# Kernel tuning notes

Hardware: AMD Instinct MI355X
Metric: run time of the kernel (lower is better)

The kernel has to match this reference:

```python
import jax, jax.numpy as jnp
import numpy as np

B, S, DIM, LW, CHUNK = 4, 4096, 512, 512, 64


def _l2n(x):
    n = jnp.sqrt(jnp.sum(x * x, axis=-1, keepdims=True))
    return x / jnp.maximum(n, 1e-12)


def setup_inputs() -> dict:
    key = jax.random.key(0)
    k = jax.random.split(key, 10)
    s = 1.0 / np.sqrt(DIM)
    return {
        "x": jax.random.normal(k[0], (B, S, DIM), jnp.float32),
        "Wq": jax.random.normal(k[1], (DIM, DIM), jnp.float32) * s,
        "Wk": jax.random.normal(k[2], (DIM, DIM), jnp.float32) * s,
        "Wv": jax.random.normal(k[3], (DIM, DIM), jnp.float32) * s,
        "init_w1": jax.random.normal(k[4], (LW, DIM), jnp.float32) * 0.02,
        "init_b1": jnp.zeros((LW,), jnp.float32),
        "init_w2": jax.random.normal(k[5], (DIM, LW), jnp.float32) * 0.02,
        "init_b2": jnp.zeros((DIM,), jnp.float32),
        "alpha_w": jax.random.normal(k[6], (DIM,), jnp.float32) * s,
        "alpha_b": jnp.full((1,), -5.0, jnp.float32),
        "eta_w": jax.random.normal(k[7], (DIM,), jnp.float32) * s,
        "eta_b": jnp.full((1,), 2.0, jnp.float32),
        "theta_w": jax.random.normal(k[8], (DIM,), jnp.float32) * s,
        "theta_b": jnp.full((1,), -4.6, jnp.float32),
        "chunk_size": CHUNK,
    }


def reference(x, Wq, Wk, Wv, init_w1, init_b1, init_w2, init_b2,
              alpha_w, alpha_b, eta_w, eta_b, theta_w, theta_b, chunk_size):
    b, s, d = x.shape
    c = int(chunk_size)
    nC = s // c
    lw = init_w1.shape[0]
    # per-sample memory params (broadcast of shared init) + zero momentum
    w1 = jnp.broadcast_to(init_w1, (b, lw, d))
    b1 = jnp.broadcast_to(init_b1, (b, lw))
    w2 = jnp.broadcast_to(init_w2, (b, d, lw))
    b2 = jnp.broadcast_to(init_b2, (b, d))
    mom = (jnp.zeros_like(w1), jnp.zeros_like(b1), jnp.zeros_like(w2), jnp.zeros_like(b2))
    xc = x.reshape(b, nC, c, d).transpose(1, 0, 2, 3)  # [nC, B, C, D]

    def step(carry, x_c):
        (w1, b1, w2, b2), (mw1, mb1, mw2, mb2) = carry
        q = _l2n(x_c @ Wq.T)
        k_ = _l2n(x_c @ Wk.T)
        v = x_c @ Wv.T
        # gates per token -> chunk-averaged, [B]
        a = jax.nn.sigmoid(x_c @ alpha_w + alpha_b).mean(axis=1)
        e = jax.nn.sigmoid(x_c @ eta_w + eta_b).mean(axis=1)
        t = jax.nn.sigmoid(x_c @ theta_w + theta_b).mean(axis=1)
        # retrieval with stale (chunk-constant) memory params
        hq = jax.nn.silu(jnp.einsum('bcd,bhd->bch', q, w1) + b1[:, None, :])
        y = jnp.einsum('bch,bdh->bcd', hq, w2) + b2[:, None, :]
        # per-token grads of mse(mlp(k), v) (mean over feature dim), chunk-averaged.
        # Analytic grads == autodiff of the tiny MLP; avoids [B,C,LW,D] intermediates.
        pre = jnp.einsum('bcd,bhd->bch', k_, w1) + b1[:, None, :]
        sg = jax.nn.sigmoid(pre)
        hk = pre * sg  # silu
        vp = jnp.einsum('bch,bdh->bcd', hk, w2) + b2[:, None, :]
        dvp = 2.0 * (vp - v) / d  # dL/d vp for mse over feature dim
        g_b2 = dvp.mean(axis=1)
        g_w2 = jnp.einsum('bcd,bch->bdh', dvp, hk) / c
        dh = jnp.einsum('bcd,bdh->bch', dvp, w2) * (sg * (1.0 + pre * (1.0 - sg)))
        g_b1 = dh.mean(axis=1)
        g_w1 = jnp.einsum('bch,bcd->bhd', dh, k_) / c
        a3, e3, t3 = a[:, None, None], e[:, None, None], t[:, None, None]
        a2, e2, t2 = a[:, None], e[:, None], t[:, None]
        nmw1 = e3 * mw1 - t3 * g_w1
        nmb1 = e2 * mb1 - t2 * g_b1
        nmw2 = e3 * mw2 - t3 * g_w2
        nmb2 = e2 * mb2 - t2 * g_b2
        nw1 = (1.0 - a3) * w1 + nmw1
        nb1 = (1.0 - a2) * b1 + nmb1
        nw2 = (1.0 - a3) * w2 + nmw2
        nb2 = (1.0 - a2) * b2 + nmb2
        return ((nw1, nb1, nw2, nb2), (nmw1, nmb1, nmw2, nmb2)), y

    _, ys = jax.lax.scan(step, ((w1, b1, w2, b2), mom), xc)
    return ys.transpose(1, 0, 2, 3).reshape(b, s, d)
```

## Files before the change

### kernel.cpp

```cpp
#include <hip/hip_runtime.h>
#include <hip/hip_bf16.h>

#define BB 4
#define SS 4096
#define DD 512
#define LWW 512
#define CC 64
#define NCH 64

typedef unsigned short u16;
using fragAB = __attribute__((ext_vector_type(8))) short;
using fragC  = __attribute__((ext_vector_type(4))) float;
using u16x4  = __attribute__((ext_vector_type(4))) short;

__device__ __forceinline__ short f2bf(float f){
  unsigned u = __float_as_uint(f);
  u = (u + 0x7FFFu + ((u >> 16) & 1u)) >> 16;
  return (short)u;
}
__device__ __forceinline__ float bf2f(short s){
  return __uint_as_float(((unsigned)(u16)s) << 16);
}
__device__ __forceinline__ fragC zeroC(){ fragC z = {0.f,0.f,0.f,0.f}; return z; }

__device__ __forceinline__ fragAB frag_bf16g(const u16* __restrict__ base, int ld, int r0, int k0, int lane){
  return *(const fragAB*)(base + (size_t)(r0 + (lane & 15)) * ld + k0 + ((lane >> 4) << 3));
}
__device__ __forceinline__ fragAB frag_lds(const short* base, int ld, int r0, int k0, int lane){
  return *(const fragAB*)(base + (r0 + (lane & 15)) * ld + k0 + ((lane >> 4) << 3));
}
#define MFMA16(a,b,c) __builtin_amdgcn_mfma_f32_16x16x32_bf16(a,b,c,0,0,0)

__device__ __forceinline__ void ld_sys(fragAB& r, const u16* p){
  asm volatile("global_load_dwordx4 %0, %1, off sc0 sc1" : "=v"(r) : "v"(p) : "memory");
}
__device__ __forceinline__ void st_sys8(u16* p, u16x4 v){
  asm volatile("global_store_dwordx2 %0, %1, off sc0 sc1" :: "v"(p), "v"(v) : "memory");
}
__device__ __forceinline__ void st_sys16(u16* p, fragAB v){
  asm volatile("global_store_dwordx4 %0, %1, off sc0 sc1" :: "v"(p), "v"(v) : "memory");
}
#define WAITVM(N) do { asm volatile("s_waitcnt vmcnt(" #N ")" ::: "memory"); \
                       __builtin_amdgcn_sched_barrier(0); } while (0)

__device__ __forceinline__ const u16* taddr(const u16* base, int c, int kq){
  return base + (((size_t)((kq >> 4)*64 + c)) << 4) + (kq & 15);
}

__device__ __forceinline__ void bar_arrive(unsigned* slots, unsigned phase, int tl){
  asm volatile("s_waitcnt vmcnt(0)" ::: "memory");
  __builtin_amdgcn_sched_barrier(0);
  __syncthreads();
  if (threadIdx.x == 0)
    __hip_atomic_store(slots + (size_t)tl*32, phase, __ATOMIC_RELAXED, __HIP_MEMORY_SCOPE_AGENT);
}
__device__ __forceinline__ void bar_wait(unsigned* slots, unsigned phase){
  if (threadIdx.x < 64){
    bool mine = threadIdx.x < 32;
    unsigned* sp = slots + (size_t)(threadIdx.x & 31)*32;
    for (;;){
      unsigned v = mine ? __hip_atomic_load(sp, __ATOMIC_RELAXED, __HIP_MEMORY_SCOPE_AGENT) : phase;
      if (__all((int)(v >= phase))) break;
      __builtin_amdgcn_s_sleep(1);
    }
  }
  __syncthreads();
}

__global__ __launch_bounds__(256) void k_cvt(const float* __restrict__ x,
    const float* __restrict__ Wq, const float* __restrict__ Wk, const float* __restrict__ Wv,
    u16* __restrict__ xb, u16* __restrict__ Wc, unsigned* __restrict__ bar){
  size_t i = (size_t)blockIdx.x * 256 + threadIdx.x;
  if (blockIdx.x == 0){
    for (int z = threadIdx.x; z < 4096; z += 256) bar[z] = 0u;
  }
  const size_t NX4 = (size_t)BB*SS*DD/4;
  const size_t NW4 = (size_t)DD*DD/4;
  if (i < NX4){
    float4 v = ((const float4*)x)[i];
    u16x4 o = { f2bf(v.x), f2bf(v.y), f2bf(v.z), f2bf(v.w) };
    *(u16x4*)(xb + 4*i) = o;
  } else if (i < NX4 + 3*NW4){
    size_t j = i - NX4;
    const float* src = (j < NW4) ? Wq : (j < 2*NW4) ? Wk : Wv;
    size_t jj = j % NW4;
    float4 v = ((const float4*)src)[jj];
    u16x4 o = { f2bf(v.x), f2bf(v.y), f2bf(v.z), f2bf(v.w) };
    *(u16x4*)(Wc + 4*j) = o;
  }
}

__global__ __launch_bounds__(256) void k_proj(const u16* __restrict__ xb,
    const u16* __restrict__ Wc,
    u16* __restrict__ Qb, u16* __restrict__ Kb, float* __restrict__ V){
  int mt = blockIdx.x / 12, nt = blockIdx.x % 12;
  int lane = threadIdx.x & 63, wid = threadIdx.x >> 6;
  int m0 = mt * 64 + wid * 16;
  const u16* Bp = Wc + (size_t)nt * 128 * DD;
  fragC acc[8];
#pragma unroll
  for (int i = 0; i < 8; ++i) acc[i] = zeroC();
  for (int k0 = 0; k0 < DD; k0 += 32){
    fragAB a = frag_bf16g(xb, DD, m0, k0, lane);
#pragma unroll
    for (int nf = 0; nf < 8; ++nf)
      acc[nf] = MFMA16(a, frag_bf16g(Bp, DD, nf*16, k0, lane), acc[nf]);
  }
#pragma unroll
  for (int nf = 0; nf < 8; ++nf){
#pragma unroll
    for (int r = 0; r < 4; ++r){
      int m = m0 + ((lane >> 4) << 2) + r;
      int col = nt*128 + nf*16 + (lane & 15);
      float v = acc[nf][r];
      if (nt < 4)      Qb[(size_t)m*DD + col]        = (u16)f2bf(v);
      else if (nt < 8) Kb[(size_t)m*DD + col - 512]  = (u16)f2bf(v);
      else             V [(size_t)m*DD + col - 1024] = v;
    }
  }
}

__global__ __launch_bounds__(256) void k_norm(u16* __restrict__ Qb, u16* __restrict__ Kb){
  int idx = blockIdx.x * 4 + (threadIdx.x >> 6);
  int lane = threadIdx.x & 63;
  u16* p = (idx < BB*SS ? Qb + (size_t)idx * DD
                        : Kb + (size_t)(idx - BB*SS) * DD) + lane * 8;
  fragAB v = *(const fragAB*)p;
  float f[8]; float s = 0.f;
#pragma unroll
  for (int i = 0; i < 8; ++i){ f[i] = bf2f(v[i]); s += f[i]*f[i]; }
#pragma unroll
  for (int o = 32; o > 0; o >>= 1) s += __shfl_xor(s, o, 64);
  float inv = 1.f / fmaxf(sqrtf(s), 1e-12f);
  fragAB o8;
#pragma unroll
  for (int i = 0; i < 8; ++i) o8[i] = f2bf(f[i] * inv);
  *(fragAB*)p = o8;
}

__global__ __launch_bounds__(256) void k_trans(const u16* __restrict__ Kb, u16* __restrict__ KT){
  __shared__ short tile[64][68];
  int blk = blockIdx.x;
  int b = blk >> 9, rem = blk & 511;
  int st = rem >> 3, dt = rem & 7;
  int s0 = st*64, d0 = dt*64;
  int sr = threadIdx.x & 63, q = threadIdx.x >> 6;
  const u16* src = Kb + ((size_t)b*SS + s0 + sr)*DD + d0 + q*16;
  fragAB v0 = *(const fragAB*)src;
  fragAB v1 = *(const fragAB*)(src + 8);
#pragma unroll
  for (int i = 0; i < 8; ++i){ tile[sr][q*16+i] = v0[i]; tile[sr][q*16+8+i] = v1[i]; }
  __syncthreads();
  fragAB o0, o1;
#pragma unroll
  for (int i = 0; i < 8; ++i){ o0[i] = tile[q*16+i][sr]; o1[i] = tile[q*16+8+i][sr]; }
  u16* dst = KT + ((size_t)b*DD + d0 + sr)*SS + s0 + q*16;
  *(fragAB*)dst = o0;
  *(fragAB*)(dst + 8) = o1;
}

__global__ __launch_bounds__(256) void k_gates(const float* __restrict__ x,
    const float* __restrict__ aw, const float* __restrict__ ab,
    const float* __restrict__ ew, const float* __restrict__ eb,
    const float* __restrict__ tw, const float* __restrict__ tb,
    float* __restrict__ aet){
  __shared__ float part[64][4][3];
  __shared__ float rowsig[64][3];
  int b = blockIdx.x >> 6, t = blockIdx.x & 63;
  int tid = threadIdx.x;
  int r = tid >> 2, p = tid & 3;
  const float4* xp = (const float4*)(x + ((size_t)b*SS + (size_t)t*CC + r) * DD + p * 128);
  const float4* a4 = (const float4*)(aw + p*128);
  const float4* e4 = (const float4*)(ew + p*128);
  const float4* t4 = (const float4*)(tw + p*128);
  float s0 = 0.f, s1 = 0.f, s2 = 0.f;
  for (int i = 0; i < 32; ++i){
    float4 xv = xp[i], av = a4[i], ev = e4[i], tv = t4[i];
    s0 += xv.x*av.x + xv.y*av.y + xv.z*av.z + xv.w*av.w;
    s1 += xv.x*ev.x + xv.y*ev.y + xv.z*ev.z + xv.w*ev.w;
    s2 += xv.x*tv.x + xv.y*tv.y + xv.z*tv.z + xv.w*tv.w;
  }
  part[r][p][0] = s0; part[r][p][1] = s1; part[r][p][2] = s2;
  __syncthreads();
  if (tid < 64){
    float a_ = part[tid][0][0]+part[tid][1][0]+part[tid][2][0]+part[tid][3][0] + ab[0];
    float e_ = part[tid][0][1]+part[tid][1][1]+part[tid][2][1]+part[tid][3][1] + eb[0];
    float t_ = part[tid][0][2]+part[tid][1][2]+part[tid][2][2]+part[tid][3][2] + tb[0];
    rowsig[tid][0] = 1.f/(1.f+expf(-a_));
    rowsig[tid][1] = 1.f/(1.f+expf(-e_));
    rowsig[tid][2] = 1.f/(1.f+expf(-t_));
  }
  __syncthreads();
  if (tid < 3){
    float s = 0.f;
    for (int i = 0; i < 64; ++i) s += rowsig[i][tid];
    aet[((size_t)b*NCH + t)*3 + tid] = s * (1.f/64.f);
  }
}

__global__ __launch_bounds__(512, 2) void k_scan(
    const u16* __restrict__ Qb, const u16* __restrict__ Kb, const u16* __restrict__ KTg,
    const float* __restrict__ V, const float* __restrict__ aet,
    const float* __restrict__ iw1, const float* __restrict__ ib1,
    const float* __restrict__ iw2, const float* __restrict__ ib2,
    u16* __restrict__ hkb, u16* __restrict__ hqs, u16* __restrict__ hkT,
    u16* __restrict__ dvpb, u16* __restrict__ w2Tb,
    float* __restrict__ out, unsigned* __restrict__ barb)
{
  __shared__ __align__(16) short s_w1[16*520];
  __shared__ __align__(16) short s_w2[16*520];
  __shared__ __align__(16) short s_pf[16*520];
  __shared__ __align__(16) short s_t[16*72];
  __shared__ __align__(16) short s_hk[64*16];
  __shared__ __align__(16) short s_hq[64*16];
  __shared__ float s_part[64][17];
  __shared__ float s_b1[16], s_mb1[16], s_b2[16], s_mb2[16];

  const int tid  = threadIdx.x;
  const int lane = tid & 63;
  const int wid  = tid >> 6;
  const int q    = lane >> 4;
  const int l15  = lane & 15;
  const int qk   = q << 3;
  const int b    = (blockIdx.x & 7) >> 1;
  const int tl   = ((blockIdx.x >> 3) << 1) | (blockIdx.x & 1);
  const int h0   = tl * 16;
  const int d0   = tl * 16;
  unsigned* slots = barb + (size_t)b * 1024;
  unsigned  ph   = 0;

  const u16* Kball = Kb  + (size_t)b*SS*DD;
  const u16* Qball = Qb  + (size_t)b*SS*DD;
  const u16* KTbat = KTg + (size_t)b*DD*SS;
  u16* hk_b  = hkb  + (size_t)b*CC*LWW;
  u16* hq_b  = hqs  + (size_t)b*CC*LWW;
  u16* hkT_b = hkT  + (size_t)b*LWW*CC;
  u16* dv_b  = dvpb + (size_t)b*CC*DD;
  const size_t W2TBUF = (size_t)BB*DD*LWW;

  float w1f[16], mw1f[16], w2f[16], mw2f[16], actr[4];

  {
    u16* w2T0 = w2Tb + (size_t)b*DD*LWW;
#pragma unroll
    for (int nf = 0; nf < 4; ++nf){
      u16x4 pk;
#pragma unroll
      for (int r = 0; r < 4; ++r){
        int hr = q*4 + r;
        int dcol = wid*64 + nf*16 + l15;
        float a = iw1[(size_t)(h0 + hr)*DD + dcol];
        w1f[nf*4+r] = a; mw1f[nf*4+r] = 0.f;
        s_w1[hr*520 + dcol] = f2bf(a);
        float c = iw2[(size_t)(d0 + hr)*LWW + dcol];
        w2f[nf*4+r] = c; mw2f[nf*4+r] = 0.f;
        s_w2[hr*520 + dcol] = f2bf(c);
        pk[r] = f2bf(c);
      }
      st_sys8(w2T0 + (size_t)(wid*64 + nf*16 + l15)*DD + d0 + q*4, pk);
    }
    if (tid < 16){
      s_b1[tid] = ib1[h0 + tid]; s_mb1[tid] = 0.f;
      s_b2[tid] = ib2[d0 + tid]; s_mb2[tid] = 0.f;
    }
#pragma unroll
    for (int r = 0; r < 4; ++r) actr[r] = 0.f;
    WAITVM(0);
    __syncthreads();
  }

  for (int t = 0; t < NCH; ++t){
    if (t > 0){
      fragAB kfr[8];
      {
        const u16* KTm = KTbat + (size_t)(t-1)*CC;
#pragma unroll
        for (int nf = 0; nf < 4; ++nf)
#pragma unroll
          for (int kk = 0; kk < 2; ++kk)
            kfr[nf*2+kk] = frag_bf16g(KTm, SS, wid*64 + nf*16, kk*32, lane);
      }
      {
        const int cst = (wid & 3) * 16;
        const int kh  = (wid >> 2) * 256;
        fragAB fa[8];
        fragC a0 = zeroC();
#pragma unroll
        for (int j = 0; j < 8; ++j) ld_sys(fa[j], taddr(dv_b, cst + l15, kh + j*32 + qk));
        WAITVM(4);
#pragma unroll
        for (int j = 0; j < 4; ++j) a0 = MFMA16(fa[j], frag_lds(s_pf, 520, 0, kh + j*32, lane), a0);
        WAITVM(0);
#pragma unroll
        for (int j = 4; j < 8; ++j) a0 = MFMA16(fa[j], frag_lds(s_pf, 520, 0, kh + j*32, lane), a0);
        if (wid >= 4){
#pragma unroll
          for (int r = 0; r < 4; ++r) s_part[cst + q*4 + r][l15] = a0[r];
        }
        __syncthreads();
        if (wid < 4){
#pragma unroll
          for (int r = 0; r < 4; ++r){
            float v = (a0[r] + s_part[cst + q*4 + r][l15]) * actr[r];
            s_t[l15*72 + cst + q*4 + r] = f2bf(v);
          }
        }
      }
      __syncthreads();
      {
        fragC ag[4];
#pragma unroll
        for (int i = 0; i < 4; ++i) ag[i] = zeroC();
#pragma unroll
        for (int kk = 0; kk < 2; ++kk){
          fragAB af = frag_lds(s_t, 72, 0, kk*32, lane);
#pragma unroll
          for (int nf = 0; nf < 4; ++nf)
            ag[nf] = MFMA16(af, kfr[nf*2+kk], ag[nf]);
        }
        const float* g3 = aet + ((size_t)b*NCH + (t-1)) * 3;
        float ga = g3[0], ge = g3[1], gth = g3[2];
#pragma unroll
        for (int nf = 0; nf < 4; ++nf)
#pragma unroll
          for (int r = 0; r < 4; ++r){
            float g  = ag[nf][r] * (1.f/64.f);
            float m_ = ge*mw1f[nf*4+r] - gth*g;
            float w_ = (1.f-ga)*w1f[nf*4+r] + m_;
            mw1f[nf*4+r] = m_; w1f[nf*4+r] = w_;
            s_w1[(q*4+r)*520 + wid*64 + nf*16 + l15] = f2bf(w_);
          }
        if (tid < 16){
          const fragAB* row = (const fragAB*)(s_t + tid*72);
          float s = 0.f;
#pragma unroll
          for (int j = 0; j < 8; ++j){
            fragAB v = row[j];
#pragma unroll
            for (int i = 0; i < 8; ++i) s += bf2f(v[i]);
          }
          float gb = s * (1.f/64.f);
          float m_ = ge*s_mb1[tid] - gth*gb;
          float bn = (1.f-ga)*s_b1[tid] + m_;
          s_mb1[tid] = m_; s_b1[tid] = bn;
        }
      }
    }
    __syncthreads();
    {
      const u16* Ac = (wid < 4 ? Kball : Qball) + (size_t)t*CC*DD;
      int m0 = (wid & 3) * 16;
      fragC acc = zeroC();
      for (int k0 = 0; k0 < DD; k0 += 32)
        acc = MFMA16(frag_bf16g(Ac, DD, m0, k0, lane),
                     frag_lds(s_w1, 520, 0, k0, lane), acc);
      float bb = s_b1[l15];
      if (wid < 4){
#pragma unroll
        for (int r = 0; r < 4; ++r){
          int c = m0 + q*4 + r;
          float pre = acc[r] + bb;
          float sg  = 1.f/(1.f+expf(-pre));
          float hkv = pre * sg;
          actr[r]   = sg * (1.f + pre * (1.f - sg));
          short hb  = f2bf(hkv);
          s_hk[c*16 + l15] = hb;
          s_t[l15*72 + c]  = hb;
        }
      } else {
#pragma unroll
        for (int r = 0; r < 4; ++r){
          int c = m0 + q*4 + r;
          float hqv = acc[r] + bb;
          float s2  = 1.f/(1.f+expf(-hqv));
          s_hq[c*16 + l15] = f2bf(hqv * s2);
        }
      }
    }
    __syncthreads();
    if (tid < 128){
      st_sys16(hk_b + (size_t)tl*1024 + tid*8, *(const fragAB*)(s_hk + tid*8));
    } else if (tid < 256){
      int i = tid - 128;
      st_sys16(hq_b + (size_t)tl*1024 + i*8, *(const fragAB*)(s_hq + i*8));
    } else if (tid < 384){
      int i = tid - 256;
      int row = i >> 3, seg = i & 7;
      st_sys16(hkT_b + (size_t)(h0 + row)*CC + seg*8, *(const fragAB*)(s_t + row*72 + seg*8));
    }
    ph++; bar_arrive(slots, ph, tl);
    bar_wait(slots, ph);

    {
      const u16* Ah = (wid < 4) ? hq_b : hk_b;
      int m0 = (wid & 3) * 16;
      fragC acc = zeroC();
      fragAB va[4], vb[4], hfr[8];
      float vv[4];
      if (wid >= 4){
#pragma unroll
        for (int r = 0; r < 4; ++r)
          vv[r] = V[((size_t)b*SS + (size_t)t*CC + m0 + q*4 + r)*DD + d0 + l15];
      }
#pragma unroll
      for (int j = 0; j < 4; ++j) ld_sys(va[j], taddr(Ah, m0 + l15, j*32 + qk));
#pragma unroll
      for (int j = 0; j < 4; ++j) ld_sys(vb[j], taddr(Ah, m0 + l15, 128 + j*32 + qk));
      WAITVM(4);
#pragma unroll
      for (int j = 0; j < 4; ++j) acc = MFMA16(va[j], frag_lds(s_w2, 520, 0, j*32, lane), acc);
#pragma unroll
      for (int j = 0; j < 4; ++j) ld_sys(va[j], taddr(Ah, m0 + l15, 256 + j*32 + qk));
      WAITVM(4);
#pragma unroll
      for (int j = 0; j < 4; ++j) acc = MFMA16(vb[j], frag_lds(s_w2, 520, 0, 128 + j*32, lane), acc);
#pragma unroll
      for (int j = 0; j < 4; ++j) ld_sys(vb[j], taddr(Ah, m0 + l15, 384 + j*32 + qk));
      WAITVM(4);
#pragma unroll
      for (int j = 0; j < 4; ++j) acc = MFMA16(va[j], frag_lds(s_w2, 520, 0, 256 + j*32, lane), acc);
#pragma unroll
      for (int nf = 0; nf < 4; ++nf)
#pragma unroll
        for (int kk = 0; kk < 2; ++kk)
          ld_sys(hfr[nf*2+kk], hkT_b + (size_t)(wid*64 + nf*16 + l15)*CC + kk*32 + qk);
      WAITVM(8);
#pragma unroll
      for (int j = 0; j < 4; ++j) acc = MFMA16(vb[j], frag_lds(s_w2, 520, 0, 384 + j*32, lane), acc);

      float bb = s_b2[l15];
      if (wid < 4){
#pragma unroll
        for (int r = 0; r < 4; ++r){
          int c = m0 + q*4 + r;
          __builtin_nontemporal_store(acc[r] + bb,
            &out[((size_t)b*SS + (size_t)t*CC + c)*DD + d0 + l15]);
        }
      } else {
#pragma unroll
        for (int r = 0; r < 4; ++r){
          int c = m0 + q*4 + r;
          float dvv = (acc[r] + bb - vv[r]) * (2.f/512.f);
          short db_ = f2bf(dvv);
          s_hk[c*16 + l15] = db_;
          s_t[l15*72 + c]  = db_;
        }
      }
      __syncthreads();
      if (tid < 128)
        st_sys16(dv_b + (size_t)tl*1024 + tid*8, *(const fragAB*)(s_hk + tid*8));
      ph++; bar_arrive(slots, ph, tl);
      {
        fragC ag[4];
#pragma unroll
        for (int i = 0; i < 4; ++i) ag[i] = zeroC();
#pragma unroll
        for (int kk = 0; kk < 2; ++kk){
          fragAB af = frag_lds(s_t, 72, 0, kk*32, lane);
#pragma unroll
          for (int nf = 0; nf < 4; ++nf)
            ag[nf] = MFMA16(af, hfr[nf*2+kk], ag[nf]);
        }
        fragAB t0, t1;
        int hr = tid >> 5;
        int c0 = (tid & 31) << 4;
        if (t + 1 < NCH){
          const u16* w2Tp = w2Tb + (size_t)(t&1)*W2TBUF + (size_t)b*DD*LWW;
          const u16* src = w2Tp + (size_t)(h0 + hr)*DD + c0;
          ld_sys(t0, src);
          ld_sys(t1, src + 8);
        }
        const float* g3 = aet + ((size_t)b*NCH + t) * 3;
        float ga = g3[0], ge = g3[1], gth = g3[2];
        u16* w2Tn = w2Tb + (size_t)((t+1)&1)*W2TBUF + (size_t)b*DD*LWW;
#pragma unroll
        for (int nf = 0; nf < 4; ++nf){
          u16x4 pk;
#pragma unroll
          for (int r = 0; r < 4; ++r){
            float g  = ag[nf][r] * (1.f/64.f);
            float m_ = ge*mw2f[nf*4+r] - gth*g;
            float w_ = (1.f-ga)*w2f[nf*4+r] + m_;
            mw2f[nf*4+r] = m_; w2f[nf*4+r] = w_;
            short wb = f2bf(w_);
            s_w2[(q*4+r)*520 + wid*64 + nf*16 + l15] = wb;
            pk[r] = wb;
          }
          st_sys8(w2Tn + (size_t)(wid*64 + nf*16 + l15)*DD + d0 + q*4, pk);
        }
        if (tid < 16){
          const fragAB* row = (const fragAB*)(s_t + tid*72);
          float s = 0.f;
#pragma unroll
          for (int j = 0; j < 8; ++j){
            fragAB v = row[j];
#pragma unroll
            for (int i = 0; i < 8; ++i) s += bf2f(v[i]);
          }
          float gb = s * (1.f/64.f);
          float m_ = ge*s_mb2[tid] - gth*gb;
          float bn = (1.f-ga)*s_b2[tid] + m_;
          s_mb2[tid] = m_; s_b2[tid] = bn;
        }
        if (t + 1 < NCH){
          WAITVM(0);
          *(fragAB*)(s_pf + hr*520 + c0)     = t0;
          *(fragAB*)(s_pf + hr*520 + c0 + 8) = t1;
        }
      }
      bar_wait(slots, ph);
    }
  }
}

extern "C" void kernel_launch(void* const* d_in, const int* in_sizes, int n_in,
                              void* d_out, int out_size, void* d_ws, size_t ws_size,
                              hipStream_t stream){
  const float* x   = (const float*)d_in[0];
  const float* Wq  = (const float*)d_in[1];
  const float* Wk  = (const float*)d_in[2];
  const float* Wv  = (const float*)d_in[3];
  const float* iw1 = (const float*)d_in[4];
  const float* ib1 = (const float*)d_in[5];
  const float* iw2 = (const float*)d_in[6];
  const float* ib2 = (const float*)d_in[7];
  const float* aw  = (const float*)d_in[8];
  const float* ab  = (const float*)d_in[9];
  const float* ew  = (const float*)d_in[10];
  const float* eb  = (const float*)d_in[11];
  const float* tw  = (const float*)d_in[12];
  const float* tb  = (const float*)d_in[13];
  float* out = (float*)d_out;

  float* fw = (float*)d_ws;
  float* V    = fw;  fw += (size_t)BB*SS*DD;
  float* aet  = fw;  fw += (size_t)BB*NCH*3 + 64;
  unsigned* bar = (unsigned*)fw; fw += 4096;
  u16* xb   = (u16*)fw;
  u16* Wc   = xb   + (size_t)BB*SS*DD;
  u16* Qb   = Wc   + (size_t)3*DD*DD;
  u16* Kb   = Qb   + (size_t)BB*SS*DD;
  u16* hkb  = Kb   + (size_t)BB*SS*DD;
  u16* hqs  = hkb  + (size_t)BB*CC*LWW;
  u16* hkT  = hqs  + (size_t)BB*CC*LWW;
  u16* dvpb = hkT  + (size_t)BB*LWW*CC;
  u16* w2Tb = dvpb + (size_t)BB*CC*DD;
  u16* KTg  = xb;

  k_cvt  <<<8960, 256, 0, stream>>>(x, Wq, Wk, Wv, xb, Wc, bar);
  k_proj <<<3072, 256, 0, stream>>>(xb, Wc, Qb, Kb, V);
  k_norm <<<8192, 256, 0, stream>>>(Qb, Kb);
  k_trans<<<2048, 256, 0, stream>>>(Kb, KTg);
  k_gates<<<256,  256, 0, stream>>>(x, aw, ab, ew, eb, tw, tb, aet);
  k_scan <<<128,  512, 0, stream>>>(Qb, Kb, KTg, V, aet, iw1, ib1, iw2, ib2,
                                    hkb, hqs, hkT, dvpb, w2Tb, out, bar);
}
```

Before: 1.357 ms.

## Interleave two batches per scan block to hide grid-barrier latency

Each persistent scan block now handles the same hidden/feature tile for two batch elements instead of one, halving the grid to 64 blocks with 1 block per CU. Phases for the two batches are interleaved so that one batch's grid-barrier wait overlaps with the other batch's compute. Weights are duplicated in dynamic shared memory. The trade-off is more registers per thread and fewer blocks to spread across CUs, in exchange for hiding the cross-block synchronisation latency of the sequential scan.

```diff
diff --git a/kernel.cpp b/kernel.cpp
--- a/kernel.cpp
+++ b/kernel.cpp
@@ -7,6 +7,7 @@
 #define LWW 512
 #define CC 64
 #define NCH 64
+#define SCAN_SMEM 111104
 
 typedef unsigned short u16;
 using fragAB = __attribute__((ext_vector_type(8))) short;
@@ -198,7 +199,296 @@
   }
 }
 
-__global__ __launch_bounds__(512, 2) void k_scan(
+struct BCtx {
+  const u16 *Kball, *Qball, *KTbat;
+  u16 *hk_b, *hq_b, *hkT_b, *dv_b, *w2T_b;
+  const float *V_b, *aet_b;
+  float *out_b;
+  unsigned *slots;
+  short *s_w1, *s_w2, *s_pf;
+  float *s_b1, *s_mb1, *s_b2, *s_mb2;
+};
+
+__device__ __forceinline__ void do_init(const BCtx& C,
+    const float* iw1, const float* ib1, const float* iw2, const float* ib2,
+    int tid, int wid, int q, int l15, int h0,
+    float (&w1f)[16], float (&mw1f)[16], float (&w2f)[16], float (&mw2f)[16],
+    float (&actr)[4])
+{
+#pragma unroll
+  for (int nf = 0; nf < 4; ++nf){
+    u16x4 pk;
+#pragma unroll
+    for (int r = 0; r < 4; ++r){
+      int hr = q*4 + r;
+      int dcol = wid*64 + nf*16 + l15;
+      float a = iw1[(size_t)(h0 + hr)*DD + dcol];
+      w1f[nf*4+r] = a; mw1f[nf*4+r] = 0.f;
+      C.s_w1[hr*520 + dcol] = f2bf(a);
+      float c = iw2[(size_t)(h0 + hr)*LWW + dcol];
+      w2f[nf*4+r] = c; mw2f[nf*4+r] = 0.f;
+      C.s_w2[hr*520 + dcol] = f2bf(c);
+      pk[r] = f2bf(c);
+    }
+    st_sys8(C.w2T_b + (size_t)(wid*64 + nf*16 + l15)*DD + h0 + q*4, pk);
+  }
+  if (tid < 16){
+    C.s_b1[tid] = ib1[h0 + tid]; C.s_mb1[tid] = 0.f;
+    C.s_b2[tid] = ib2[h0 + tid]; C.s_mb2[tid] = 0.f;
+  }
+#pragma unroll
+  for (int r = 0; r < 4; ++r) actr[r] = 0.f;
+}
+
+__device__ __forceinline__ void do_phaseA(const BCtx& C, int t,
+    int tid, int lane, int wid, int q, int l15, int qk, int tl, int h0,
+    float (&w1f)[16], float (&mw1f)[16], float (&actr)[4],
+    short* s_t, short* s_hk, short* s_hq, float (*s_part)[17], unsigned phA)
+{
+  if (t > 0){
+    fragAB kfr[8];
+    {
+      const u16* KTm = C.KTbat + (size_t)(t-1)*CC;
+#pragma unroll
+      for (int nf = 0; nf < 4; ++nf)
+#pragma unroll
+        for (int kk = 0; kk < 2; ++kk)
+          kfr[nf*2+kk] = frag_bf16g(KTm, SS, wid*64 + nf*16, kk*32, lane);
+    }
+    {
+      const int cst = (wid & 3) * 16;
+      const int kh  = (wid >> 2) * 256;
+      fragAB fa[8];
+      fragC a0 = zeroC();
+#pragma unroll
+      for (int j = 0; j < 8; ++j) ld_sys(fa[j], taddr(C.dv_b, cst + l15, kh + j*32 + qk));
+      WAITVM(4);
+#pragma unroll
+      for (int j = 0; j < 4; ++j) a0 = MFMA16(fa[j], frag_lds(C.s_pf, 520, 0, kh + j*32, lane), a0);
+      WAITVM(0);
+#pragma unroll
+      for (int j = 4; j < 8; ++j) a0 = MFMA16(fa[j], frag_lds(C.s_pf, 520, 0, kh + j*32, lane), a0);
+      if (wid >= 4){
+#pragma unroll
+        for (int r = 0; r < 4; ++r) s_part[cst + q*4 + r][l15] = a0[r];
+      }
+      __syncthreads();
+      if (wid < 4){
+#pragma unroll
+        for (int r = 0; r < 4; ++r){
+          float v = (a0[r] + s_part[cst + q*4 + r][l15]) * actr[r];
+          s_t[l15*72 + cst + q*4 + r] = f2bf(v);
+        }
+      }
+      __syncthreads();
+    }
+    {
+      fragC ag[4];
+#pragma unroll
+      for (int i = 0; i < 4; ++i) ag[i] = zeroC();
+#pragma unroll
+      for (int kk = 0; kk < 2; ++kk){
+        fragAB af = frag_lds(s_t, 72, 0, kk*32, lane);
+#pragma unroll
+        for (int nf = 0; nf < 4; ++nf)
+          ag[nf] = MFMA16(af, kfr[nf*2+kk], ag[nf]);
+      }
+      const float* g3 = C.aet_b + (size_t)(t-1)*3;
+      float ga = g3[0], ge = g3[1], gth = g3[2];
+#pragma unroll
+      for (int nf = 0; nf < 4; ++nf)
+#pragma unroll
+        for (int r = 0; r < 4; ++r){
+          float g  = ag[nf][r] * (1.f/64.f);
+          float m_ = ge*mw1f[nf*4+r] - gth*g;
+          float w_ = (1.f-ga)*w1f[nf*4+r] + m_;
+          mw1f[nf*4+r] = m_; w1f[nf*4+r] = w_;
+          C.s_w1[(q*4+r)*520 + wid*64 + nf*16 + l15] = f2bf(w_);
+        }
+      if (tid < 16){
+        const fragAB* row = (const fragAB*)(s_t + tid*72);
+        float s = 0.f;
+#pragma unroll
+        for (int j = 0; j < 8; ++j){
+          fragAB v = row[j];
+#pragma unroll
+          for (int i = 0; i < 8; ++i) s += bf2f(v[i]);
+        }
+        float gb = s * (1.f/64.f);
+        float m_ = ge*C.s_mb1[tid] - gth*gb;
+        float bn = (1.f-ga)*C.s_b1[tid] + m_;
+        C.s_mb1[tid] = m_; C.s_b1[tid] = bn;
+      }
+    }
+  }
+  __syncthreads();
+  {
+    const u16* Ac = (wid < 4 ? C.Kball : C.Qball) + (size_t)t*CC*DD;
+    int m0 = (wid & 3) * 16;
+    fragC acc = zeroC();
+    for (int k0 = 0; k0 < DD; k0 += 32)
+      acc = MFMA16(frag_bf16g(Ac, DD, m0, k0, lane),
+                   frag_lds(C.s_w1, 520, 0, k0, lane), acc);
+    float bb = C.s_b1[l15];
+    if (wid < 4){
+#pragma unroll
+      for (int r = 0; r < 4; ++r){
+        int c = m0 + q*4 + r;
+        float pre = acc[r] + bb;
+        float sg  = 1.f/(1.f+expf(-pre));
+        float hkv = pre * sg;
+        actr[r]   = sg * (1.f + pre * (1.f - sg));
+        short hb  = f2bf(hkv);
+        s_hk[c*16 + l15] = hb;
+        s_t[l15*72 + c]  = hb;
+      }
+    } else {
+#pragma unroll
+      for (int r = 0; r < 4; ++r){
+        int c = m0 + q*4 + r;
+        float hqv = acc[r] + bb;
+        float s2  = 1.f/(1.f+expf(-hqv));
+        s_hq[c*16 + l15] = f2bf(hqv * s2);
+      }
+    }
+  }
+  __syncthreads();
+  if (tid < 128){
+    st_sys16(C.hk_b + (size_t)tl*1024 + tid*8, *(const fragAB*)(s_hk + tid*8));
+  } else if (tid < 256){
+    int i = tid - 128;
+    st_sys16(C.hq_b + (size_t)tl*1024 + i*8, *(const fragAB*)(s_hq + i*8));
+  } else if (tid < 384){
+    int i = tid - 256;
+    int row = i >> 3, seg = i & 7;
+    st_sys16(C.hkT_b + (size_t)(h0 + row)*CC + seg*8, *(const fragAB*)(s_t + row*72 + seg*8));
+  }
+  bar_arrive(C.slots, phA, tl);
+}
+
+__device__ __forceinline__ void do_phaseB(const BCtx& C, int t,
+    int tid, int lane, int wid, int q, int l15, int qk, int tl, int d0,
+    float (&w2f)[16], float (&mw2f)[16],
+    short* s_t, short* s_hk, unsigned phB, size_t W2TBUF)
+{
+  const u16* Ah = (wid < 4) ? C.hq_b : C.hk_b;
+  int m0 = (wid & 3) * 16;
+  fragC acc = zeroC();
+  fragAB va[4], vb[4], hfr[8];
+  float vv[4];
+  if (wid >= 4){
+#pragma unroll
+    for (int r = 0; r < 4; ++r)
+      vv[r] = C.V_b[((size_t)t*CC + m0 + q*4 + r)*DD + d0 + l15];
+  }
+#pragma unroll
+  for (int j = 0; j < 4; ++j) ld_sys(va[j], taddr(Ah, m0 + l15, j*32 + qk));
+#pragma unroll
+  for (int j = 0; j < 4; ++j) ld_sys(vb[j], taddr(Ah, m0 + l15, 128 + j*32 + qk));
+  WAITVM(4);
+#pragma unroll
+  for (int j = 0; j < 4; ++j) acc = MFMA16(va[j], frag_lds(C.s_w2, 520, 0, j*32, lane), acc);
+#pragma unroll
+  for (int j = 0; j < 4; ++j) ld_sys(va[j], taddr(Ah, m0 + l15, 256 + j*32 + qk));
+  WAITVM(4);
+#pragma unroll
+  for (int j = 0; j < 4; ++j) acc = MFMA16(vb[j], frag_lds(C.s_w2, 520, 0, 128 + j*32, lane), acc);
+#pragma unroll
+  for (int j = 0; j < 4; ++j) ld_sys(vb[j], taddr(Ah, m0 + l15, 384 + j*32 + qk));
+  WAITVM(4);
+#pragma unroll
+  for (int j = 0; j < 4; ++j) acc = MFMA16(va[j], frag_lds(C.s_w2, 520, 0, 256 + j*32, lane), acc);
+#pragma unroll
+  for (int nf = 0; nf < 4; ++nf)
+#pragma unroll
+    for (int kk = 0; kk < 2; ++kk)
+      ld_sys(hfr[nf*2+kk], C.hkT_b + (size_t)(wid*64 + nf*16 + l15)*CC + kk*32 + qk);
+  WAITVM(8);
+#pragma unroll
+  for (int j = 0; j < 4; ++j) acc = MFMA16(vb[j], frag_lds(C.s_w2, 520, 0, 384 + j*32, lane), acc);
+
+  float bb = C.s_b2[l15];
+  if (wid < 4){
+#pragma unroll
+    for (int r = 0; r < 4; ++r){
+      int c = m0 + q*4 + r;
+      __builtin_nontemporal_store(acc[r] + bb, &C.out_b[((size_t)t*CC + c)*DD + d0 + l15]);
+    }
+  } else {
+#pragma unroll
+    for (int r = 0; r < 4; ++r){
+      int c = m0 + q*4 + r;
+      float dvv = (acc[r] + bb - vv[r]) * (2.f/512.f);
+      short db_ = f2bf(dvv);
+      s_hk[c*16 + l15] = db_;
+      s_t[l15*72 + c]  = db_;
+    }
+  }
+  __syncthreads();
+  if (tid < 128)
+    st_sys16(C.dv_b + (size_t)tl*1024 + tid*8, *(const fragAB*)(s_hk + tid*8));
+  bar_arrive(C.slots, phB, tl);
+  {
+    fragC ag[4];
+#pragma unroll
+    for (int i = 0; i < 4; ++i) ag[i] = zeroC();
+#pragma unroll
+    for (int kk = 0; kk < 2; ++kk){
+      fragAB af = frag_lds(s_t, 72, 0, kk*32, lane);
+#pragma unroll
+      for (int nf = 0; nf < 4; ++nf)
+        ag[nf] = MFMA16(af, hfr[nf*2+kk], ag[nf]);
+    }
+    fragAB t0, t1;
+    int hr = tid >> 5;
+    int c0 = (tid & 31) << 4;
+    if (t + 1 < NCH){
+      const u16* w2Tp = C.w2T_b + (size_t)(t&1)*W2TBUF;
+      const u16* src = w2Tp + (size_t)(d0 + hr)*DD + c0;
+      ld_sys(t0, src);
+      ld_sys(t1, src + 8);
+    }
+    const float* g3 = C.aet_b + (size_t)t*3;
+    float ga = g3[0], ge = g3[1], gth = g3[2];
+    u16* w2Tn = C.w2T_b + (size_t)((t+1)&1)*W2TBUF;
+#pragma unroll
+    for (int nf = 0; nf < 4; ++nf){
+      u16x4 pk;
+#pragma unroll
+      for (int r = 0; r < 4; ++r){
+        float g  = ag[nf][r] * (1.f/64.f);
+        float m_ = ge*mw2f[nf*4+r] - gth*g;
+        float w_ = (1.f-ga)*w2f[nf*4+r] + m_;
+        mw2f[nf*4+r] = m_; w2f[nf*4+r] = w_;
+        short wb = f2bf(w_);
+        C.s_w2[(q*4+r)*520 + wid*64 + nf*16 + l15] = wb;
+        pk[r] = wb;
+      }
+      st_sys8(w2Tn + (size_t)(wid*64 + nf*16 + l15)*DD + d0 + q*4, pk);
+    }
+    if (tid < 16){
+      const fragAB* row = (const fragAB*)(s_t + tid*72);
+      float s = 0.f;
+#pragma unroll
+      for (int j = 0; j < 8; ++j){
+        fragAB v = row[j];
+#pragma unroll
+        for (int i = 0; i < 8; ++i) s += bf2f(v[i]);
+      }
+      float gb = s * (1.f/64.f);
+      float m_ = ge*C.s_mb2[tid] - gth*gb;
+      float bn = (1.f-ga)*C.s_b2[tid] + m_;
+      C.s_mb2[tid] = m_; C.s_b2[tid] = bn;
+    }
+    if (t + 1 < NCH){
+      WAITVM(0);
+      *(fragAB*)(C.s_pf + hr*520 + c0)     = t0;
+      *(fragAB*)(C.s_pf + hr*520 + c0 + 8) = t1;
+    }
+  }
+}
+
+__global__ __launch_bounds__(512, 1) void k_scan(
     const u16* __restrict__ Qb, const u16* __restrict__ Kb, const u16* __restrict__ KTg,
     const float* __restrict__ V, const float* __restrict__ aet,
     const float* __restrict__ iw1, const float* __restrict__ ib1,
@@ -207,14 +497,23 @@
     u16* __restrict__ dvpb, u16* __restrict__ w2Tb,
     float* __restrict__ out, unsigned* __restrict__ barb)
 {
-  __shared__ __align__(16) short s_w1[16*520];
-  __shared__ __align__(16) short s_w2[16*520];
-  __shared__ __align__(16) short s_pf[16*520];
-  __shared__ __align__(16) short s_t[16*72];
-  __shared__ __align__(16) short s_hk[64*16];
-  __shared__ __align__(16) short s_hq[64*16];
-  __shared__ float s_part[64][17];
-  __shared__ float s_b1[16], s_mb1[16], s_b2[16], s_mb2[16];
+  extern __shared__ __align__(16) char smem_raw[];
+  short* sp = (short*)smem_raw;
+  short* s_w1a = sp;               sp += 16*520;
+  short* s_w2a = sp;               sp += 16*520;
+  short* s_pfa = sp;               sp += 16*520;
+  short* s_w1b = sp;               sp += 16*520;
+  short* s_w2b = sp;               sp += 16*520;
+  short* s_pfb = sp;               sp += 16*520;
+  short* s_t   = sp;               sp += 16*72;
+  short* s_hk  = sp;               sp += 64*16;
+  short* s_hq  = sp;               sp += 64*16;
+  float* fb = (float*)sp;
+  float (*s_part)[17] = (float(*)[17])fb;  fb += 64*17;
+  float* s_b1a = fb;  fb += 16;  float* s_mb1a = fb; fb += 16;
+  float* s_b2a = fb;  fb += 16;  float* s_mb2a = fb; fb += 16;
+  float* s_b1b = fb;  fb += 16;  float* s_mb1b = fb; fb += 16;
+  float* s_b2b = fb;  fb += 16;  float* s_mb2b = fb; fb += 16;
 
   const int tid  = threadIdx.x;
   const int lane = tid & 63;
@@ -222,295 +521,56 @@
   const int q    = lane >> 4;
   const int l15  = lane & 15;
   const int qk   = q << 3;
-  const int b    = (blockIdx.x & 7) >> 1;
-  const int tl   = ((blockIdx.x >> 3) << 1) | (blockIdx.x & 1);
+  const int g    = blockIdx.x & 1;
+  const int tl   = blockIdx.x >> 1;
   const int h0   = tl * 16;
-  const int d0   = tl * 16;
-  unsigned* slots = barb + (size_t)b * 1024;
-  unsigned  ph   = 0;
-
-  const u16* Kball = Kb  + (size_t)b*SS*DD;
-  const u16* Qball = Qb  + (size_t)b*SS*DD;
-  const u16* KTbat = KTg + (size_t)b*DD*SS;
-  u16* hk_b  = hkb  + (size_t)b*CC*LWW;
-  u16* hq_b  = hqs  + (size_t)b*CC*LWW;
-  u16* hkT_b = hkT  + (size_t)b*LWW*CC;
-  u16* dv_b  = dvpb + (size_t)b*CC*DD;
+  const int b0   = g*2, b1 = g*2 + 1;
   const size_t W2TBUF = (size_t)BB*DD*LWW;
 
-  float w1f[16], mw1f[16], w2f[16], mw2f[16], actr[4];
-
+  BCtx C0, C1;
   {
-    u16* w2T0 = w2Tb + (size_t)b*DD*LWW;
-#pragma unroll
-    for (int nf = 0; nf < 4; ++nf){
-      u16x4 pk;
-#pragma unroll
-      for (int r = 0; r < 4; ++r){
-        int hr = q*4 + r;
-        int dcol = wid*64 + nf*16 + l15;
-        float a = iw1[(size_t)(h0 + hr)*DD + dcol];
-        w1f[nf*4+r] = a; mw1f[nf*4+r] = 0.f;
-        s_w1[hr*520 + dcol] = f2bf(a);
-        float c = iw2[(size_t)(d0 + hr)*LWW + dcol];
-        w2f[nf*4+r] = c; mw2f[nf*4+r] = 0.f;
-        s_w2[hr*520 + dcol] = f2bf(c);
-        pk[r] = f2bf(c);
-      }
-      st_sys8(w2T0 + (size_t)(wid*64 + nf*16 + l15)*DD + d0 + q*4, pk);
-    }
-    if (tid < 16){
-      s_b1[tid] = ib1[h0 + tid]; s_mb1[tid] = 0.f;
-      s_b2[tid] = ib2[d0 + tid]; s_mb2[tid] = 0.f;
-    }
-#pragma unroll
-    for (int r = 0; r < 4; ++r) actr[r] = 0.f;
-    WAITVM(0);
-    __syncthreads();
-  }
+    C0.Kball = Kb + (size_t)b0*SS*DD;  C1.Kball = Kb + (size_t)b1*SS*DD;
+    C0.Qball = Qb + (size_t)b0*SS*DD;  C1.Qball = Qb + (size_t)b1*SS*DD;
+    C0.KTbat = KTg + (size_t)b0*DD*SS; C1.KTbat = KTg + (size_t)b1*DD*SS;
+    C0.hk_b  = hkb + (size_t)b0*CC*LWW;  C1.hk_b  = hkb + (size_t)b1*CC*LWW;
+    C0.hq_b  = hqs + (size_t)b0*CC*LWW;  C1.hq_b  = hqs + (size_t)b1*CC*LWW;
+    C0.hkT_b = hkT + (size_t)b0*LWW*CC;  C1.hkT_b = hkT + (size_t)b1*LWW*CC;
+    C0.dv_b  = dvpb + (size_t)b0*CC*DD;  C1.dv_b  = dvpb + (size_t)b1*CC*DD;
+    C0.w2T_b = w2Tb + (size_t)b0*DD*LWW; C1.w2T_b = w2Tb + (size_t)b1*DD*LWW;
+    C0.V_b   = V + (size_t)b0*SS*DD;     C1.V_b   = V + (size_t)b1*SS*DD;
+    C0.aet_b = aet + (size_t)b0*NCH*3;   C1.aet_b = aet + (size_t)b1*NCH*3;
+    C0.out_b = out + (size_t)b0*SS*DD;   C1.out_b = out + (size_t)b1*SS*DD;
+    C0.slots = barb + (size_t)b0*1024;   C1.slots = barb + (size_t)b1*1024;
+    C0.s_w1 = s_w1a; C0.s_w2 = s_w2a; C0.s_pf = s_pfa;
+    C1.s_w1 = s_w1b; C1.s_w2 = s_w2b; C1.s_pf = s_pfb;
+    C0.s_b1 = s_b1a; C0.s_mb1 = s_mb1a; C0.s_b2 = s_b2a; C0.s_mb2 = s_mb2a;
+    C1.s_b1 = s_b1b; C1.s_mb1 = s_mb1b; C1.s_b2 = s_b2b; C1.s_mb2 = s_mb2b;
+  }
+
+  float w1f0[16], mw1f0[16], w2f0[16], mw2f0[16], actr0[4];
+  float w1f1[16], mw1f1[16], w2f1[16], mw2f1[16], actr1[4];
+
+  do_init(C0, iw1, ib1, iw2, ib2, tid, wid, q, l15, h0, w1f0, mw1f0, w2f0, mw2f0, actr0);
+  do_init(C1, iw1, ib1, iw2, ib2, tid, wid, q, l15, h0, w1f1, mw1f1, w2f1, mw2f1, actr1);
+  WAITVM(0);
+  __syncthreads();
 
   for (int t = 0; t < NCH; ++t){
-    if (t > 0){
-      fragAB kfr[8];
-      {
-        const u16* KTm = KTbat + (size_t)(t-1)*CC;
-#pragma unroll
-        for (int nf = 0; nf < 4; ++nf)
-#pragma unroll
-          for (int kk = 0; kk < 2; ++kk)
-            kfr[nf*2+kk] = frag_bf16g(KTm, SS, wid*64 + nf*16, kk*32, lane);
-      }
-      {
-        const int cst = (wid & 3) * 16;
-        const int kh  = (wid >> 2) * 256;
-        fragAB fa[8];
-        fragC a0 = zeroC();
-#pragma unroll
-        for (int j = 0; j < 8; ++j) ld_sys(fa[j], taddr(dv_b, cst + l15, kh + j*32 + qk));
-        WAITVM(4);
-#pragma unroll
-        for (int j = 0; j < 4; ++j) a0 = MFMA16(fa[j], frag_lds(s_pf, 520, 0, kh + j*32, lane), a0);
-        WAITVM(0);
-#pragma unroll
-        for (int j = 4; j < 8; ++j) a0 = MFMA16(fa[j], frag_lds(s_pf, 520, 0, kh + j*32, lane), a0);
-        if (wid >= 4){
-#pragma unroll
-          for (int r = 0; r < 4; ++r) s_part[cst + q*4 + r][l15] = a0[r];
-        }
-        __syncthreads();
-        if (wid < 4){
-#pragma unroll
-          for (int r = 0; r < 4; ++r){
-            float v = (a0[r] + s_part[cst + q*4 + r][l15]) * actr[r];
-            s_t[l15*72 + cst + q*4 + r] = f2bf(v);
-          }
-        }
-      }
-      __syncthreads();
-      {
-        fragC ag[4];
-#pragma unroll
-        for (int i = 0; i < 4; ++i) ag[i] = zeroC();
-#pragma unroll
-        for (int kk = 0; kk < 2; ++kk){
-          fragAB af = frag_lds(s_t, 72, 0, kk*32, lane);
-#pragma unroll
-          for (int nf = 0; nf < 4; ++nf)
-            ag[nf] = MFMA16(af, kfr[nf*2+kk], ag[nf]);
-        }
-        const float* g3 = aet + ((size_t)b*NCH + (t-1)) * 3;
-        float ga = g3[0], ge = g3[1], gth = g3[2];
-#pragma unroll
-        for (int nf = 0; nf < 4; ++nf)
-#pragma unroll
-          for (int r = 0; r < 4; ++r){
-            float g  = ag[nf][r] * (1.f/64.f);
-            float m_ = ge*mw1f[nf*4+r] - gth*g;
-            float w_ = (1.f-ga)*w1f[nf*4+r] + m_;
-            mw1f[nf*4+r] = m_; w1f[nf*4+r] = w_;
-            s_w1[(q*4+r)*520 + wid*64 + nf*16 + l15] = f2bf(w_);
-          }
-        if (tid < 16){
-          const fragAB* row = (const fragAB*)(s_t + tid*72);
-          float s = 0.f;
-#pragma unroll
-          for (int j = 0; j < 8; ++j){
-            fragAB v = row[j];
-#pragma unroll
-            for (int i = 0; i < 8; ++i) s += bf2f(v[i]);
-          }
-          float gb = s * (1.f/64.f);
-          float m_ = ge*s_mb1[tid] - gth*gb;
-          float bn = (1.f-ga)*s_b1[tid] + m_;
-          s_mb1[tid] = m_; s_b1[tid] = bn;
-        }
-      }
-    }
-    __syncthreads();
-    {
-      const u16* Ac = (wid < 4 ? Kball : Qball) + (size_t)t*CC*DD;
-      int m0 = (wid & 3) * 16;
-      fragC acc = zeroC();
-      for (int k0 = 0; k0 < DD; k0 += 32)
-        acc = MFMA16(frag_bf16g(Ac, DD, m0, k0, lane),
-                     frag_lds(s_w1, 520, 0, k0, lane), acc);
-      float bb = s_b1[l15];
-      if (wid < 4){
-#pragma unroll
-        for (int r = 0; r < 4; ++r){
-          int c = m0 + q*4 + r;
-          float pre = acc[r] + bb;
-          float sg  = 1.f/(1.f+expf(-pre));
-          float hkv = pre * sg;
-          actr[r]   = sg * (1.f + pre * (1.f - sg));
-          short hb  = f2bf(hkv);
-          s_hk[c*16 + l15] = hb;
-          s_t[l15*72 + c]  = hb;
-        }
-      } else {
-#pragma unroll
-        for (int r = 0; r < 4; ++r){
-          int c = m0 + q*4 + r;
-          float hqv = acc[r] + bb;
-          float s2  = 1.f/(1.f+expf(-hqv));
-          s_hq[c*16 + l15] = f2bf(hqv * s2);
-        }
-      }
-    }
-    __syncthreads();
-    if (tid < 128){
-      st_sys16(hk_b + (size_t)tl*1024 + tid*8, *(const fragAB*)(s_hk + tid*8));
-    } else if (tid < 256){
-      int i = tid - 128;
-      st_sys16(hq_b + (size_t)tl*1024 + i*8, *(const fragAB*)(s_hq + i*8));
-    } else if (tid < 384){
-      int i = tid - 256;
-      int row = i >> 3, seg = i & 7;
-      st_sys16(hkT_b + (size_t)(h0 + row)*CC + seg*8, *(const fragAB*)(s_t + row*72 + seg*8));
-    }
-    ph++; bar_arrive(slots, ph, tl);
-    bar_wait(slots, ph);
-
-    {
-      const u16* Ah = (wid < 4) ? hq_b : hk_b;
-      int m0 = (wid & 3) * 16;
-      fragC acc = zeroC();
-      fragAB va[4], vb[4], hfr[8];
-      float vv[4];
-      if (wid >= 4){
-#pragma unroll
-        for (int r = 0; r < 4; ++r)
-          vv[r] = V[((size_t)b*SS + (size_t)t*CC + m0 + q*4 + r)*DD + d0 + l15];
-      }
-#pragma unroll
-      for (int j = 0; j < 4; ++j) ld_sys(va[j], taddr(Ah, m0 + l15, j*32 + qk));
-#pragma unroll
-      for (int j = 0; j < 4; ++j) ld_sys(vb[j], taddr(Ah, m0 + l15, 128 + j*32 + qk));
-      WAITVM(4);
-#pragma unroll
-      for (int j = 0; j < 4; ++j) acc = MFMA16(va[j], frag_lds(s_w2, 520, 0, j*32, lane), acc);
-#pragma unroll
-      for (int j = 0; j < 4; ++j) ld_sys(va[j], taddr(Ah, m0 + l15, 256 + j*32 + qk));
-      WAITVM(4);
-#pragma unroll
-      for (int j = 0; j < 4; ++j) acc = MFMA16(vb[j], frag_lds(s_w2, 520, 0, 128 + j*32, lane), acc);
-#pragma unroll
-      for (int j = 0; j < 4; ++j) ld_sys(vb[j], taddr(Ah, m0 + l15, 384 + j*32 + qk));
-      WAITVM(4);
-#pragma unroll
-      for (int j = 0; j < 4; ++j) acc = MFMA16(va[j], frag_lds(s_w2, 520, 0, 256 + j*32, lane), acc);
-#pragma unroll
-      for (int nf = 0; nf < 4; ++nf)
-#pragma unroll
-        for (int kk = 0; kk < 2; ++kk)
-          ld_sys(hfr[nf*2+kk], hkT_b + (size_t)(wid*64 + nf*16 + l15)*CC + kk*32 + qk);
-      WAITVM(8);
-#pragma unroll
-      for (int j = 0; j < 4; ++j) acc = MFMA16(vb[j], frag_lds(s_w2, 520, 0, 384 + j*32, lane), acc);
-
-      float bb = s_b2[l15];
-      if (wid < 4){
-#pragma unroll
-        for (int r = 0; r < 4; ++r){
-          int c = m0 + q*4 + r;
-          __builtin_nontemporal_store(acc[r] + bb,
-            &out[((size_t)b*SS + (size_t)t*CC + c)*DD + d0 + l15]);
-        }
-      } else {
-#pragma unroll
-        for (int r = 0; r < 4; ++r){
-          int c = m0 + q*4 + r;
-          float dvv = (acc[r] + bb - vv[r]) * (2.f/512.f);
-          short db_ = f2bf(dvv);
-          s_hk[c*16 + l15] = db_;
-          s_t[l15*72 + c]  = db_;
-        }
-      }
-      __syncthreads();
-      if (tid < 128)
-        st_sys16(dv_b + (size_t)tl*1024 + tid*8, *(const fragAB*)(s_hk + tid*8));
-      ph++; bar_arrive(slots, ph, tl);
-      {
-        fragC ag[4];
-#pragma unroll
-        for (int i = 0; i < 4; ++i) ag[i] = zeroC();
-#pragma unroll
-        for (int kk = 0; kk < 2; ++kk){
-          fragAB af = frag_lds(s_t, 72, 0, kk*32, lane);
-#pragma unroll
-          for (int nf = 0; nf < 4; ++nf)
-            ag[nf] = MFMA16(af, hfr[nf*2+kk], ag[nf]);
-        }
-        fragAB t0, t1;
-        int hr = tid >> 5;
-        int c0 = (tid & 31) << 4;
-        if (t + 1 < NCH){
-          const u16* w2Tp = w2Tb + (size_t)(t&1)*W2TBUF + (size_t)b*DD*LWW;
-          const u16* src = w2Tp + (size_t)(h0 + hr)*DD + c0;
-          ld_sys(t0, src);
-          ld_sys(t1, src + 8);
-        }
-        const float* g3 = aet + ((size_t)b*NCH + t) * 3;
-        float ga = g3[0], ge = g3[1], gth = g3[2];
-        u16* w2Tn = w2Tb + (size_t)((t+1)&1)*W2TBUF + (size_t)b*DD*LWW;
-#pragma unroll
-        for (int nf = 0; nf < 4; ++nf){
-          u16x4 pk;
-#pragma unroll
-          for (int r = 0; r < 4; ++r){
-            float g  = ag[nf][r] * (1.f/64.f);
-            float m_ = ge*mw2f[nf*4+r] - gth*g;
-            float w_ = (1.f-ga)*w2f[nf*4+r] + m_;
-            mw2f[nf*4+r] = m_; w2f[nf*4+r] = w_;
-            short wb = f2bf(w_);
-            s_w2[(q*4+r)*520 + wid*64 + nf*16 + l15] = wb;
-            pk[r] = wb;
-          }
-          st_sys8(w2Tn + (size_t)(wid*64 + nf*16 + l15)*DD + d0 + q*4, pk);
-        }
-        if (tid < 16){
-          const fragAB* row = (const fragAB*)(s_t + tid*72);
-          float s = 0.f;
-#pragma unroll
-          for (int j = 0; j < 8; ++j){
-            fragAB v = row[j];
-#pragma unroll
-            for (int i = 0; i < 8; ++i) s += bf2f(v[i]);
-          }
-          float gb = s * (1.f/64.f);
-          float m_ = ge*s_mb2[tid] - gth*gb;
-          float bn = (1.f-ga)*s_b2[tid] + m_;
-          s_mb2[tid] = m_; s_b2[tid] = bn;
-        }
-        if (t + 1 < NCH){
-          WAITVM(0);
-          *(fragAB*)(s_pf + hr*520 + c0)     = t0;
-          *(fragAB*)(s_pf + hr*520 + c0 + 8) = t1;
-        }
-      }
-      bar_wait(slots, ph);
-    }
-  }
+    unsigned phA = 2u*t + 1u, phB = 2u*t + 2u;
+    do_phaseA(C0, t, tid, lane, wid, q, l15, qk, tl, h0,
+              w1f0, mw1f0, actr0, s_t, s_hk, s_hq, s_part, phA);
+    if (t > 0) bar_wait(C1.slots, 2u*t);
+    do_phaseA(C1, t, tid, lane, wid, q, l15, qk, tl, h0,
+              w1f1, mw1f1, actr1, s_t, s_hk, s_hq, s_part, phA);
+    bar_wait(C0.slots, phA);
+    do_phaseB(C0, t, tid, lane, wid, q, l15, qk, tl, h0,
+              w2f0, mw2f0, s_t, s_hk, phB, W2TBUF);
+    bar_wait(C1.slots, phA);
+    do_phaseB(C1, t, tid, lane, wid, q, l15, qk, tl, h0,
+              w2f1, mw2f1, s_t, s_hk, phB, W2TBUF);
+    bar_wait(C0.slots, phB);
+  }
+  WAITVM(0);
 }
 
 extern "C" void kernel_launch(void* const* d_in, const int* in_sizes, int n_in,
@@ -552,6 +612,6 @@
   k_norm <<<8192, 256, 0, stream>>>(Qb, Kb);
   k_trans<<<2048, 256, 0, stream>>>(Kb, KTg);
   k_gates<<<256,  256, 0, stream>>>(x, aw, ab, ew, eb, tw, tb, aet);
-  k_scan <<<128,  512, 0, stream>>>(Qb, Kb, KTg, V, aet, iw1, ib1, iw2, ib2,
-                                    hkb, hqs, hkT, dvpb, w2Tb, out, bar);
-}
+  k_scan <<<64,   512, SCAN_SMEM, stream>>>(Qb, Kb, KTg, V, aet, iw1, ib1, iw2, ib2,
+                                            hkb, hqs, hkT, dvpb, w2Tb, out, bar);
+}
```

New measurement: 3.662 ms. 170% more time.
